# Kernel tuning notes

Hardware: AMD Instinct MI355X
Metric: run time of the kernel (lower is better)

Reference implementation:

```python
import jax, jax.numpy as jnp
from jax import lax
import numpy as np

NUM_EMBEDDINGS = 8192
EMBEDDING_DIM = 256
COMMITMENT_COST = 0.25


def setup_inputs() -> dict:
    key = jax.random.key(0)
    k1, k2 = jax.random.split(key)
    z = jax.random.normal(k1, (16, EMBEDDING_DIM, 32, 32), dtype=jnp.float32)
    codebook = jax.random.uniform(
        k2, (NUM_EMBEDDINGS, EMBEDDING_DIM), dtype=jnp.float32,
        minval=-1.0 / NUM_EMBEDDINGS, maxval=1.0 / NUM_EMBEDDINGS)
    return {"z": z, "codebook": codebook}


def reference(z, codebook):
    B, C, H, W = z.shape  # C == embedding_dim
    zp = jnp.transpose(z, (0, 2, 3, 1))          # [B, H, W, C]
    z_flat = zp.reshape(-1, C)                    # [N, C], N = B*H*W
    # squared-distance via ||z||^2 + ||e||^2 - 2 z.e
    z2 = jnp.sum(z_flat * z_flat, axis=1, keepdims=True)   # [N, 1]
    e2 = jnp.sum(codebook * codebook, axis=1)               # [K]
    ez = z_flat @ codebook.T                                # [N, K]
    distances = z2 + e2 - 2.0 * ez                          # [N, K]
    e_indices = jnp.argmin(distances, axis=1)               # [N]
    z_q = codebook[e_indices]                               # [N, C]
    # Faithfully reproduce the original's mislabeled unpack:
    # torch does B, D, H, W = z.shape on the BHWC tensor, then
    # z_q.view(B, H, W, D).permute(0, 3, 1, 2) == reshape(B, W, C, H) -> (0,3,1,2)
    z_q = jnp.transpose(z_q.reshape(B, W, C, H), (0, 3, 1, 2))  # [B, H, W, C]
    commitment_loss = jnp.mean((lax.stop_gradient(zp) - z_q) ** 2)
    codebook_loss = jnp.mean((zp - lax.stop_gradient(z_q)) ** 2)
    loss = codebook_loss + COMMITMENT_COST * commitment_loss
    z_q_st = zp + lax.stop_gradient(z_q - zp)   # straight-through, [B, H, W, C]
    return z_q_st, loss, e_indices
```

## Files before the change

### kernel.cpp

```cpp
#include <hip/hip_runtime.h>
#include <stdint.h>

#define NROWS 16384
#define KENT  8192
#define CDIM  256
#define NELEM 4194304

#define ZSCALE 22.0f
#define ESCALE 1040384.0f
#define MARGIN_INT 4096
#define SBIAS 4194304


typedef int v4i __attribute__((ext_vector_type(4)));

__device__ inline int q8(float x, float s) {
    int v = __float2int_rn(x * s);
    return v < -127 ? -127 : (v > 127 ? 127 : v);
}
__device__ inline unsigned pk4(int a, int b, int c, int d) {
    return (a & 255) | ((b & 255) << 8) | ((c & 255) << 16) | ((d & 255) << 24);
}
__device__ inline unsigned umax_(unsigned a, unsigned b) { return a > b ? a : b; }
__device__ inline unsigned umin_(unsigned a, unsigned b) { return a < b ? a : b; }
__device__ inline void gload_lds16(const void* g, void* l) {
    __builtin_amdgcn_global_load_lds(
        (const __attribute__((address_space(1))) void*)g,
        (__attribute__((address_space(3))) void*)l, 16, 0, 0);
}

__global__ __launch_bounds__(128) void vq_prep(
        const float* __restrict__ z, const float* __restrict__ cb,
        float* __restrict__ z2w, char* __restrict__ zbi8,
        char* __restrict__ cbbi8, float* __restrict__ loss_out) {
    const int t = threadIdx.x;
    const int bid = blockIdx.x;

    if (bid >= 256) {
        const int p = bid - 256, n0 = p * 128;
        char* dst = cbbi8 + p * 32768;
        const float* src = cb + (n0 + t) * 256;
#pragma unroll
        for (int q = 0; q < 16; ++q) {
            float4 a = *(const float4*)(src + q * 16);
            float4 b = *(const float4*)(src + q * 16 + 4);
            float4 c = *(const float4*)(src + q * 16 + 8);
            float4 d = *(const float4*)(src + q * 16 + 12);
            uint4 v;
            v.x = pk4(q8(a.x,ESCALE), q8(a.y,ESCALE), q8(a.z,ESCALE), q8(a.w,ESCALE));
            v.y = pk4(q8(b.x,ESCALE), q8(b.y,ESCALE), q8(b.z,ESCALE), q8(b.w,ESCALE));
            v.z = pk4(q8(c.x,ESCALE), q8(c.y,ESCALE), q8(c.z,ESCALE), q8(c.w,ESCALE));
            v.w = pk4(q8(d.x,ESCALE), q8(d.y,ESCALE), q8(d.z,ESCALE), q8(d.w,ESCALE));
            *(uint4*)&dst[(q * 128 + t) * 16] = v;
        }
        if (p == 0 && t == 0) loss_out[0] = 0.f;
        return;
    }

    __shared__ float s64[64];
    const int r = t & 63;
    const int blk = t >> 6;
    const int n = bid * 64 + r;
    const int b = n >> 10, hw = n & 1023;
    const float* base = z + b * 262144 + hw;

    const int p = n >> 7, rp = n & 127;
    char* dst = zbi8 + p * 32768;

    float t0[16], p01[16], p0123[16], C[16];

#pragma unroll
    for (int j = 0; j < 8; ++j) {
        float a[16];
#pragma unroll
        for (int L = 0; L < 16; ++L)
            a[L] = base[(blk * 128 + L + 16 * j) * 1024];
        int qb[16];
#pragma unroll
        for (int L = 0; L < 16; ++L) {
            qb[L] = q8(a[L], ZSCALE);
            float sq = a[L] * a[L];
            asm volatile("" : "+v"(sq));
            if (j == 0 || j == 2 || j == 4 || j == 6) t0[L] = sq;
            else if (j == 1) p01[L] = t0[L] + sq;
            else if (j == 3) p0123[L] = p01[L] + (t0[L] + sq);
            else if (j == 5) p01[L] = t0[L] + sq;
            else             C[L] = p0123[L] + (p01[L] + (t0[L] + sq));
        }
        uint4 v;
        v.x = pk4(qb[0], qb[1], qb[2], qb[3]);
        v.y = pk4(qb[4], qb[5], qb[6], qb[7]);
        v.z = pk4(qb[8], qb[9], qb[10], qb[11]);
        v.w = pk4(qb[12], qb[13], qb[14], qb[15]);
        *(uint4*)&dst[((blk * 8 + j) * 128 + rp) * 16] = v;
    }
    float t8[8];
#pragma unroll
    for (int L = 0; L < 8; ++L) t8[L] = C[L] + C[L + 8];
    float t4[4];
#pragma unroll
    for (int L = 0; L < 4; ++L) t4[L] = t8[L] + t8[L + 4];
    float t2a = t4[0] + t4[2];
    float t2b = t4[1] + t4[3];
    float bs = t2a + t2b;

    if (blk == 1) s64[r] = bs;
    __syncthreads();
    if (blk == 0) z2w[n] = bs + s64[r];
}

__global__ __launch_bounds__(256, 4) void vq_gemm(
        const char* __restrict__ zbi8,
        const char* __restrict__ cbbi8,
        unsigned long long* __restrict__ gstats) {
    __shared__ __align__(16) char smem[32768];

    const int tid = threadIdx.x;
    const int w = tid >> 6, l = tid & 63;
    const int q4 = l >> 4, cl = l & 15;
    const int mw = w & 1, nw = w >> 1;

    const unsigned bx = blockIdx.x;
    const unsigned xcd = bx & 7, local = bx >> 3;
    const unsigned png = local >> 8;
    const unsigned rem = local & 255;
    const unsigned pm = (rem >> 4) * 8 + xcd;
    const unsigned pn = png * 16 + (rem & 15);

    const char* Ab = zbi8 + pm * 32768;
    const char* Bb = cbbi8 + pn * 32768;

#pragma unroll
    for (int u = 0; u < 8; ++u)
        gload_lds16(Ab + u * 4096 + tid * 16, smem + u * 4096 + (w << 10));

    const char* abase = Bb + (q4 * 128 + mw * 64 + cl) * 16;
    v4i af[4], afn[4];
#pragma unroll
    for (int i = 0; i < 4; ++i)
        af[i] = *(const v4i*)(abase + i * 256);

    const unsigned vb = ((unsigned)SBIAS << 6) + (unsigned)(q4 * 4);

    v4i acc[4][4];
    __syncthreads();

#pragma unroll
    for (int kt = 0; kt < 4; ++kt) {
        v4i bfl[4];
#pragma unroll
        for (int j = 0; j < 4; ++j)
            bfl[j] = *(const v4i*)(smem + kt * 8192 + q4 * 2048
                                        + nw * 1024 + j * 256 + cl * 16);
        if (kt < 3) {
#pragma unroll
            for (int i = 0; i < 4; ++i)
                afn[i] = *(const v4i*)(abase + (kt + 1) * 8192 + i * 256);
        }
#pragma unroll
        for (int i = 0; i < 4; ++i)
#pragma unroll
            for (int j = 0; j < 4; ++j) {
                if (kt == 0)
                    acc[i][j] = __builtin_amdgcn_mfma_i32_16x16x64_i8(
                        af[i], bfl[j], (v4i)0, 0, 0, 0);
                else
                    acc[i][j] = __builtin_amdgcn_mfma_i32_16x16x64_i8(
                        af[i], bfl[j], acc[i][j], 0, 0, 0);
            }
#pragma unroll
        for (int i = 0; i < 4; ++i) af[i] = afn[i];
    }

    unsigned long long* gs = gstats + (pn * 2 + (unsigned)mw) * 16384u
                                    + pm * 128u + (unsigned)(nw * 64);
#pragma unroll
    for (int jj = 0; jj < 4; ++jj) {
        unsigned m1[8], m2[8];
#pragma unroll
        for (int i = 0; i < 4; ++i)
#pragma unroll
            for (int gp = 0; gp < 2; ++gp) {
                unsigned pa = ((unsigned)acc[i][jj][2 * gp] << 6)
                              + vb + (unsigned)(i * 16 + 2 * gp);
                unsigned pb = ((unsigned)acc[i][jj][2 * gp + 1] << 6)
                              + vb + (unsigned)(i * 16 + 2 * gp + 1);
                m1[i * 2 + gp] = umax_(pa, pb);
                m2[i * 2 + gp] = umin_(pa, pb);
            }
#pragma unroll
        for (int s = 4; s >= 1; s >>= 1)
#pragma unroll
            for (int u = 0; u < 4; ++u) {
                if (u < s) {
                    unsigned a1 = m1[u], a2 = m2[u];
                    unsigned b1 = m1[u + s], b2 = m2[u + s];
                    m1[u] = umax_(a1, b1);
                    m2[u] = umax_(umin_(a1, b1), umax_(a2, b2));
                }
            }
        unsigned t1 = m1[0], t2 = m2[0];
#pragma unroll
        for (int off = 16; off <= 32; off <<= 1) {
            unsigned o1 = (unsigned)__shfl_xor((int)t1, off);
            unsigned o2 = (unsigned)__shfl_xor((int)t2, off);
            t2 = umax_(umax_(t2, o2), umin_(t1, o1));
            t1 = umax_(t1, o1);
        }
        if (q4 == 0)
            gs[jj * 16 + cl] =
                ((unsigned long long)t1 << 32) | (unsigned long long)t2;
    }
}

__global__ __launch_bounds__(256) void vq_finalize(
        const float* __restrict__ z, const float* __restrict__ cb,
        const float* __restrict__ z2w,
        const unsigned long long* __restrict__ gstats,
        float* __restrict__ out, float* __restrict__ out_idx) {
    __shared__ float zs[32][32];
    __shared__ unsigned pmax[8][32];
    __shared__ int thrL[32];
    __shared__ unsigned candL[512];
    __shared__ unsigned blkcnt;
    __shared__ unsigned long long bestL[32];
    __shared__ float tile[32 * 257];

    const int t = threadIdx.x;
    const int bid = blockIdx.x;
    const int n0 = bid * 32;
    const int b = bid >> 5, j = bid & 31;
    const int hw0 = j * 32;
    const int r = t & 31, gc = t >> 5;

    unsigned long long e[16];
    unsigned m = 0;
#pragma unroll
    for (int g2 = 0; g2 < 16; ++g2) {
        e[g2] = gstats[(size_t)(gc * 16 + g2) * 16384u + (unsigned)(n0 + r)];
        m = umax_(m, (unsigned)(e[g2] >> 32));
    }
    pmax[gc][r] = m;
    if (t == 0) blkcnt = 0;
    __syncthreads();
    if (t < 32) {
        unsigned mm = 0;
#pragma unroll
        for (int g = 0; g < 8; ++g) mm = umax_(mm, pmax[g][t]);
        thrL[t] = (int)(mm >> 6) - MARGIN_INT;
        bestL[t] = ~0ull;
    }
    __syncthreads();

    {
        int th = thrL[r];
#pragma unroll
        for (int g2 = 0; g2 < 16; ++g2) {
            unsigned p1 = (unsigned)(e[g2] >> 32), p2 = (unsigned)e[g2];
            unsigned kb = (unsigned)(gc * 16 + g2) * 64u;
            if ((int)(p1 >> 6) >= th) {
                unsigned pos = atomicAdd(&blkcnt, 1u);
                if (pos < 512u)
                    candL[pos] = ((unsigned)r << 13) | (kb + (p1 & 63u));
            }
            if ((int)(p2 >> 6) >= th) {
                unsigned pos = atomicAdd(&blkcnt, 1u);
                if (pos < 512u)
                    candL[pos] = ((unsigned)r << 13) | (kb + (p2 & 63u));
            }
        }
    }
    __syncthreads();
    int ns = (int)(blkcnt < 512u ? blkcnt : 512u);

    for (int base = 0; base < ns; base += 256) {
        bool active = base + t < ns;
        int rr0 = 0, k = 0;
        if (active) {
            unsigned v = candL[base + t];
            rr0 = v >> 13; k = v & 8191;
        }
        float sacc = 0.f;
        for (int ch = 0; ch < 8; ++ch) {
            __syncthreads();
            {
                int rr = t & 31, cc2 = t >> 5;
#pragma unroll
                for (int u = 0; u < 4; ++u) {
                    int cc = u * 8 + cc2;
                    zs[cc][rr] = z[b * 262144 + (ch * 32 + cc) * 1024 + hw0 + rr];
                }
            }
            __syncthreads();
            if (active) {
                const float4* cbp = (const float4*)(cb + k * 256 + ch * 32);
                float4 A0 = cbp[0], A1 = cbp[1], A2 = cbp[2], A3 = cbp[3];
                float4 A4 = cbp[4], A5 = cbp[5], A6 = cbp[6], A7 = cbp[7];
                float Af[32] = {A0.x,A0.y,A0.z,A0.w, A1.x,A1.y,A1.z,A1.w,
                                A2.x,A2.y,A2.z,A2.w, A3.x,A3.y,A3.z,A3.w,
                                A4.x,A4.y,A4.z,A4.w, A5.x,A5.y,A5.z,A5.w,
                                A6.x,A6.y,A6.z,A6.w, A7.x,A7.y,A7.z,A7.w};
#pragma unroll
                for (int u = 0; u < 32; ++u)
                    sacc = __builtin_fmaf(zs[u][rr0], Af[u], sacc);
            }
        }
        if (active) {
            float d = z2w[n0 + rr0] - 2.0f * sacc;
            unsigned long long key =
                ((unsigned long long)__float_as_uint(d) << 32) | (unsigned)k;
            atomicMin(&bestL[rr0], key);
        }
    }
    __syncthreads();
    if (t < 32)
        out_idx[n0 + t] = (float)(unsigned)(bestL[t] & 0xFFFFFFFFu);

    {
        const int c0 = t & 63;
        const int w0 = (t >> 6) * 8;
#pragma unroll
        for (int it = 0; it < 8; ++it) {
            int wr = w0 + it;
            int kk = (int)(unsigned)(bestL[wr] & 0xFFFFFFFFu);
            const float* src = cb + kk * 256 + c0;
            float* drow = tile + wr * 257 + c0;
            drow[0]   = src[0];
            drow[64]  = src[64];
            drow[128] = src[128];
            drow[192] = src[192];
        }
    }
    __syncthreads();

    float* obase = out + b * 262144 + j * 256;
    const int wv = t >> 3, cb8 = (t & 7) * 32;
#pragma unroll
    for (int it = 0; it < 32; ++it)
        obase[it * 8192 + t] = tile[wv * 257 + cb8 + it];
}

__global__ __launch_bounds__(256) void vq_loss(
        const float* __restrict__ z, const float* __restrict__ out,
        float* __restrict__ loss_out) {
    __shared__ float zs[256][33];
    __shared__ float wsum[4];

    const int t = threadIdx.x;
    const int b = blockIdx.x >> 5, i = blockIdx.x & 31;

#pragma unroll
    for (int it = 0; it < 32; ++it) {
        int k = it * 8 + (t >> 5);
        zs[k][t & 31] = z[b * 262144 + k * 1024 + i * 32 + (t & 31)];
    }
    __syncthreads();

    const float* ob = out + b * 262144 + i * 8192;
    float lsum = 0.f;
#pragma unroll 4
    for (int it = 0; it < 32; ++it) {
        float d = zs[t][it] - ob[it * 256 + t];
        lsum = __builtin_fmaf(d, d, lsum);
    }
#pragma unroll
    for (int off = 32; off >= 1; off >>= 1) lsum += __shfl_down(lsum, off, 64);
    int lane = t & 63, wv = t >> 6;
    if (lane == 0) wsum[wv] = lsum;
    __syncthreads();
    if (t == 0)
        atomicAdd(loss_out, (wsum[0] + wsum[1] + wsum[2] + wsum[3]) *
                            (1.25f / (float)NELEM));
}

extern "C" void kernel_launch(void* const* d_in, const int* in_sizes, int n_in,
                              void* d_out, int out_size, void* d_ws, size_t ws_size,
                              hipStream_t stream) {
    const float* z  = (const float*)d_in[0];
    const float* cb = (const float*)d_in[1];
    float* out = (float*)d_out;

    char* ws = (char*)d_ws;
    char* zbi8               = ws;
    char* cbbi8              = ws + 4194304;
    unsigned long long* gstats = (unsigned long long*)(ws + 6291456);
    float* z2w               = (float*)(ws + 23068672);

    vq_prep<<<320, 128, 0, stream>>>(z, cb, z2w, zbi8, cbbi8, out + NELEM);

    vq_gemm<<<8192, 256, 0, stream>>>(zbi8, cbbi8, gstats);

    vq_finalize<<<512, 256, 0, stream>>>(z, cb, z2w, gstats,
                                         out, out + NELEM + 1);

    vq_loss<<<512, 256, 0, stream>>>(z, out, out + NELEM);
}
```

Before: 153.0 us.

## Double prep kernel thread parallelism and raise MFMA wave priority in GEMM

The prep kernel now launches 256 threads per block instead of 128. Each z row's eight channel chunks are split across two thread halves, which combine their partial sums of squares through shared memory. The codebook quantization uses twice as many blocks, each handling 64 rows with four threads per row. The GEMM brackets its MFMA loop with s_setprio so waves issuing matrix ops get scheduling priority; this adds an extra barrier and shared-memory traffic in prep.

```diff
diff --git a/kernel.cpp b/kernel.cpp
--- a/kernel.cpp
+++ b/kernel.cpp
@@ -29,7 +29,7 @@
         (__attribute__((address_space(3))) void*)l, 16, 0, 0);
 }
 
-__global__ __launch_bounds__(128) void vq_prep(
+__global__ __launch_bounds__(256) void vq_prep(
         const float* __restrict__ z, const float* __restrict__ cb,
         float* __restrict__ z2w, char* __restrict__ zbi8,
         char* __restrict__ cbbi8, float* __restrict__ loss_out) {
@@ -37,11 +37,15 @@
     const int bid = blockIdx.x;
 
     if (bid >= 256) {
-        const int p = bid - 256, n0 = p * 128;
+        const int ppi = bid - 256;
+        const int p = ppi >> 1, h = ppi & 1;
+        const int r = t & 63, qh = t >> 6;
+        const int row = h * 64 + r;
         char* dst = cbbi8 + p * 32768;
-        const float* src = cb + (n0 + t) * 256;
-#pragma unroll
-        for (int q = 0; q < 16; ++q) {
+        const float* src = cb + (p * 128 + row) * 256;
+#pragma unroll
+        for (int qq = 0; qq < 4; ++qq) {
+            const int q = qh * 4 + qq;
             float4 a = *(const float4*)(src + q * 16);
             float4 b = *(const float4*)(src + q * 16 + 4);
             float4 c = *(const float4*)(src + q * 16 + 8);
@@ -51,15 +55,17 @@
             v.y = pk4(q8(b.x,ESCALE), q8(b.y,ESCALE), q8(b.z,ESCALE), q8(b.w,ESCALE));
             v.z = pk4(q8(c.x,ESCALE), q8(c.y,ESCALE), q8(c.z,ESCALE), q8(c.w,ESCALE));
             v.w = pk4(q8(d.x,ESCALE), q8(d.y,ESCALE), q8(d.z,ESCALE), q8(d.w,ESCALE));
-            *(uint4*)&dst[(q * 128 + t) * 16] = v;
-        }
-        if (p == 0 && t == 0) loss_out[0] = 0.f;
+            *(uint4*)&dst[(q * 128 + row) * 16] = v;
+        }
+        if (ppi == 0 && t == 0) loss_out[0] = 0.f;
         return;
     }
 
+    __shared__ float pprt[2][64][17];
     __shared__ float s64[64];
     const int r = t & 63;
-    const int blk = t >> 6;
+    const int part = t >> 6;
+    const int blk = part >> 1, jh = part & 1;
     const int n = bid * 64 + r;
     const int b = n >> 10, hw = n & 1023;
     const float* base = z + b * 262144 + hw;
@@ -67,10 +73,11 @@
     const int p = n >> 7, rp = n & 127;
     char* dst = zbi8 + p * 32768;
 
-    float t0[16], p01[16], p0123[16], C[16];
-
-#pragma unroll
-    for (int j = 0; j < 8; ++j) {
+    float t0[16], p01[16], pr[16];
+
+#pragma unroll
+    for (int jj = 0; jj < 4; ++jj) {
+        const int j = jh * 4 + jj;
         float a[16];
 #pragma unroll
         for (int L = 0; L < 16; ++L)
@@ -81,11 +88,10 @@
             qb[L] = q8(a[L], ZSCALE);
             float sq = a[L] * a[L];
             asm volatile("" : "+v"(sq));
-            if (j == 0 || j == 2 || j == 4 || j == 6) t0[L] = sq;
-            else if (j == 1) p01[L] = t0[L] + sq;
-            else if (j == 3) p0123[L] = p01[L] + (t0[L] + sq);
-            else if (j == 5) p01[L] = t0[L] + sq;
-            else             C[L] = p0123[L] + (p01[L] + (t0[L] + sq));
+            if (jj == 0)      t0[L] = sq;
+            else if (jj == 1) p01[L] = t0[L] + sq;
+            else if (jj == 2) t0[L] = sq;
+            else              pr[L] = p01[L] + (t0[L] + sq);
         }
         uint4 v;
         v.x = pk4(qb[0], qb[1], qb[2], qb[3]);
@@ -94,19 +100,30 @@
         v.w = pk4(qb[12], qb[13], qb[14], qb[15]);
         *(uint4*)&dst[((blk * 8 + j) * 128 + rp) * 16] = v;
     }
-    float t8[8];
-#pragma unroll
-    for (int L = 0; L < 8; ++L) t8[L] = C[L] + C[L + 8];
-    float t4[4];
-#pragma unroll
-    for (int L = 0; L < 4; ++L) t4[L] = t8[L] + t8[L + 4];
-    float t2a = t4[0] + t4[2];
-    float t2b = t4[1] + t4[3];
-    float bs = t2a + t2b;
-
-    if (blk == 1) s64[r] = bs;
-    __syncthreads();
-    if (blk == 0) z2w[n] = bs + s64[r];
+
+    if (jh == 1) {
+#pragma unroll
+        for (int L = 0; L < 16; ++L) pprt[blk][r][L] = pr[L];
+    }
+    __syncthreads();
+    float bs = 0.f;
+    if (jh == 0) {
+        float C[16];
+#pragma unroll
+        for (int L = 0; L < 16; ++L) C[L] = pr[L] + pprt[blk][r][L];
+        float t8[8];
+#pragma unroll
+        for (int L = 0; L < 8; ++L) t8[L] = C[L] + C[L + 8];
+        float t4[4];
+#pragma unroll
+        for (int L = 0; L < 4; ++L) t4[L] = t8[L] + t8[L + 4];
+        float t2a = t4[0] + t4[2];
+        float t2b = t4[1] + t4[3];
+        bs = t2a + t2b;
+        if (blk == 1) s64[r] = bs;
+    }
+    __syncthreads();
+    if (part == 0) z2w[n] = bs + s64[r];
 }
 
 __global__ __launch_bounds__(256, 4) void vq_gemm(
@@ -157,6 +174,7 @@
             for (int i = 0; i < 4; ++i)
                 afn[i] = *(const v4i*)(abase + (kt + 1) * 8192 + i * 256);
         }
+        __builtin_amdgcn_s_setprio(1);
 #pragma unroll
         for (int i = 0; i < 4; ++i)
 #pragma unroll
@@ -168,6 +186,7 @@
                     acc[i][j] = __builtin_amdgcn_mfma_i32_16x16x64_i8(
                         af[i], bfl[j], acc[i][j], 0, 0, 0);
             }
+        __builtin_amdgcn_s_setprio(0);
 #pragma unroll
         for (int i = 0; i < 4; ++i) af[i] = afn[i];
     }
@@ -386,7 +405,7 @@
     unsigned long long* gstats = (unsigned long long*)(ws + 6291456);
     float* z2w               = (float*)(ws + 23068672);
 
-    vq_prep<<<320, 128, 0, stream>>>(z, cb, z2w, zbi8, cbbi8, out + NELEM);
+    vq_prep<<<384, 256, 0, stream>>>(z, cb, z2w, zbi8, cbbi8, out + NELEM);
 
     vq_gemm<<<8192, 256, 0, stream>>>(zbi8, cbbi8, gstats);
 
```

After: 147.3 us. -3.7%, faster.
